# Kernel tuning notes

Measured on AMD Instinct MI355X. Metric: run time of the kernel, lower is better.

## Reference

```python
import jax, jax.numpy as jnp
import numpy as np

N = 100000   # num nodes
E = 500000   # num edges
F_IN = 128   # num_feats
H = 128      # dim_hidden
C = 40       # num_classes


def _glorot(key, fan_in, fan_out):
    lim = np.sqrt(6.0 / (fan_in + fan_out)).astype(np.float32)
    return jax.random.uniform(key, (fan_in, fan_out), jnp.float32, -lim, lim)


def setup_inputs() -> dict:
    key = jax.random.key(0)
    ks = jax.random.split(key, 8)
    x = jax.random.normal(ks[0], (N, F_IN), dtype=jnp.float32)
    edge_index = jax.random.randint(ks[1], (2, E), 0, N, dtype=jnp.int32)
    dims = [F_IN, H, H, H, C]  # num_layers = 4
    inp = {"x": x, "edge_index": edge_index}
    for i in range(4):
        inp[f"W{i}"] = _glorot(ks[2 + i], dims[i], dims[i + 1])
        inp[f"b{i}"] = jnp.zeros((dims[i + 1],), jnp.float32)
    return inp


def _gcn_norm(edge_index, num_nodes):
    # PyG gcn_norm: add self-loops (weight 1), symmetric D^-1/2 A D^-1/2
    loops = jnp.arange(num_nodes, dtype=edge_index.dtype)
    src = jnp.concatenate([edge_index[0], loops])
    dst = jnp.concatenate([edge_index[1], loops])
    deg = jax.ops.segment_sum(jnp.ones_like(src, jnp.float32), dst,
                              num_segments=num_nodes)
    dinv = jnp.where(deg > 0, jax.lax.rsqrt(deg), 0.0)
    norm = dinv[src] * dinv[dst]  # [E + N]
    return src, dst, norm


def _gcn_conv(h, W, b, src, dst, norm, num_nodes):
    h = h @ W                               # [N, out]
    msg = h[src] * norm[:, None]            # gather + scale, [E+N, out]
    agg = jax.ops.segment_sum(msg, dst, num_segments=num_nodes)
    return agg + b


def reference(x, edge_index, W0, b0, W1, b1, W2, b2, W3, b3):
    # eval mode: feature dropout and edge dropout (dropout_adj) are identity;
    # type_norm='None' -> no batchnorm.
    src, dst, norm = _gcn_norm(edge_index, N)
    Ws = [W0, W1, W2, W3]
    bs = [b0, b1, b2, b3]
    h = x
    for i in range(3):  # num_layers - 1 hidden layers with ReLU
        h = jax.nn.relu(_gcn_conv(h, Ws[i], bs[i], src, dst, norm, N))
    return _gcn_conv(h, Ws[3], bs[3], src, dst, norm, N)  # [N, C]
```

## Files before the change

kernel.cpp:

```cpp
#include <hip/hip_runtime.h>
#include <hip/hip_bf16.h>


#define F_DIM 128

#define SCAN_T 256
#define SCAN_I 8
#define SCAN_CHUNK (SCAN_T * SCAN_I)

typedef __attribute__((ext_vector_type(8))) short short8;
typedef __attribute__((ext_vector_type(4))) float f32x4;

__device__ __forceinline__ unsigned short f2bf_rne(float f) {
    unsigned int u = __float_as_uint(f);
    unsigned int r = (u + 0x7fffu + ((u >> 16) & 1u)) >> 16;
    return (unsigned short)r;
}

__global__ void count_dst_kernel(const int* __restrict__ dst, int* __restrict__ count, int E) {
    int e = blockIdx.x * blockDim.x + threadIdx.x;
    if (e < E) atomicAdd(&count[dst[e]], 1);
}

__global__ __launch_bounds__(SCAN_T) void scan_partial_kernel(const int* __restrict__ count,
                                                              int* __restrict__ blocksum, int n) {
    int b = blockIdx.x, t = threadIdx.x;
    int base = b * SCAN_CHUNK + t * SCAN_I;
    int s = 0;
#pragma unroll
    for (int j = 0; j < SCAN_I; ++j) {
        int i = base + j;
        if (i < n) s += count[i] + 1;
    }
    __shared__ int red[SCAN_T];
    red[t] = s;
    __syncthreads();
    for (int off = SCAN_T / 2; off > 0; off >>= 1) {
        if (t < off) red[t] += red[t + off];
        __syncthreads();
    }
    if (t == 0) blocksum[b] = red[0];
}

__global__ __launch_bounds__(1024) void scan_sums_kernel(const int* __restrict__ blocksum,
                                                         int* __restrict__ blockoff, int nb) {
    __shared__ int sums[1024];
    int t = threadIdx.x;
    sums[t] = (t < nb) ? blocksum[t] : 0;
    __syncthreads();
    for (int off = 1; off < 1024; off <<= 1) {
        int v = (t >= off) ? sums[t - off] : 0;
        __syncthreads();
        sums[t] += v;
        __syncthreads();
    }
    if (t < nb) blockoff[t] = (t == 0) ? 0 : sums[t - 1];
    if (t == 0) blockoff[nb] = sums[nb - 1];
}

__global__ __launch_bounds__(SCAN_T) void scan_write_fused_kernel(const int* __restrict__ count,
                                                                  const int* __restrict__ blockoff,
                                                                  int* __restrict__ rowptr,
                                                                  int* __restrict__ writepos,
                                                                  float* __restrict__ dinv,
                                                                  int* __restrict__ col,
                                                                  float* __restrict__ val,
                                                                  int n, int nb) {
    int b = blockIdx.x, t = threadIdx.x;
    int base = b * SCAN_CHUNK + t * SCAN_I;
    int c[SCAN_I];
    int s = 0;
#pragma unroll
    for (int j = 0; j < SCAN_I; ++j) {
        int i = base + j;
        c[j] = (i < n) ? count[i] + 1 : 0;
        s += c[j];
    }
    __shared__ int sums[SCAN_T];
    sums[t] = s;
    __syncthreads();
    for (int off = 1; off < SCAN_T; off <<= 1) {
        int v = (t >= off) ? sums[t - off] : 0;
        __syncthreads();
        sums[t] += v;
        __syncthreads();
    }
    int offset = blockoff[b] + ((t == 0) ? 0 : sums[t - 1]);
#pragma unroll
    for (int j = 0; j < SCAN_I; ++j) {
        int i = base + j;
        if (i < n) {
            rowptr[i] = offset;
            float d = rsqrtf((float)c[j]);
            dinv[i] = d;
            col[offset] = i;
            val[offset] = d * d;
            writepos[i] = offset + 1;
            offset += c[j];
        }
    }
    if (b == 0 && t == 0) rowptr[n] = blockoff[nb];
}

__global__ void fill_edges_kernel(const int* __restrict__ src, const int* __restrict__ dst,
                                  int* __restrict__ writepos, int* __restrict__ col,
                                  float* __restrict__ val, const float* __restrict__ dinv, int E) {
    int e = blockIdx.x * blockDim.x + threadIdx.x;
    if (e < E) {
        int s = src[e], d = dst[e];
        int p = atomicAdd(&writepos[d], 1);
        col[p] = s;
        val[p] = dinv[s] * dinv[d];
    }
}

__global__ __launch_bounds__(256) void cvt_bf16_kernel(const float* __restrict__ in,
                                                       unsigned short* __restrict__ out,
                                                       long nChunks) {
    long idx = (long)blockIdx.x * 256 + threadIdx.x;
    if (idx >= nChunks) return;
    const float4* in4 = (const float4*)in;
    float4 a = in4[idx * 2];
    float4 b = in4[idx * 2 + 1];
    uint4 o;
    o.x = (unsigned)f2bf_rne(a.x) | ((unsigned)f2bf_rne(a.y) << 16);
    o.y = (unsigned)f2bf_rne(a.z) | ((unsigned)f2bf_rne(a.w) << 16);
    o.z = (unsigned)f2bf_rne(b.x) | ((unsigned)f2bf_rne(b.y) << 16);
    o.w = (unsigned)f2bf_rne(b.z) | ((unsigned)f2bf_rne(b.w) << 16);
    ((uint4*)out)[idx] = o;
}

__global__ __launch_bounds__(256) void cvt_wt_kernel(const float* __restrict__ W,
                                                     unsigned short* __restrict__ WT) {
    int t = blockIdx.x * 256 + threadIdx.x;
    int k = t >> 7, c = t & 127;
    WT[(size_t)c * 128 + k] = f2bf_rne(W[(size_t)k * 128 + c]);
}

__global__ __launch_bounds__(256) void cvt_wt3_kernel(const float* __restrict__ W3,
                                                      unsigned short* __restrict__ WT3) {
    int t = blockIdx.x * 256 + threadIdx.x;
    if (t >= 48 * 128) return;
    int c = t >> 7, k = t & 127;
    WT3[(size_t)c * 128 + k] = (c < 40) ? f2bf_rne(W3[(size_t)k * 40 + c]) : (unsigned short)0;
}

__device__ __forceinline__ void acc8_bf16(float* acc, uint4 u, float v) {
    unsigned w[4] = {u.x, u.y, u.z, u.w};
#pragma unroll
    for (int i = 0; i < 4; ++i) {
        float lo = __uint_as_float(w[i] << 16);
        float hi = __uint_as_float(w[i] & 0xffff0000u);
        acc[2 * i] += v * lo;
        acc[2 * i + 1] += v * hi;
    }
}

__device__ __forceinline__ void gather_phase1(const int* __restrict__ rowptr,
                                              const int* __restrict__ col,
                                              const float* __restrict__ val,
                                              const uint4* __restrict__ H16,
                                              unsigned short (*aggb)[136], int n) {
    int m = threadIdx.x >> 3;
    int p = threadIdx.x & 7;
    int node = blockIdx.x * 32 + m;
    float acc[16];
#pragma unroll
    for (int q = 0; q < 16; ++q) acc[q] = 0.f;
    if (node < n) {
        int s = rowptr[node], e = rowptr[node + 1];
        int j = s;
        for (; j + 1 < e; j += 2) {
            int c0 = col[j], c1 = col[j + 1];
            float v0 = val[j], v1 = val[j + 1];
            const uint4* r0 = H16 + (size_t)c0 * 16 + p;
            const uint4* r1 = H16 + (size_t)c1 * 16 + p;
            uint4 a0 = r0[0], a1 = r0[8];
            uint4 b0 = r1[0], b1 = r1[8];
            acc8_bf16(acc + 0, a0, v0);
            acc8_bf16(acc + 8, a1, v0);
            acc8_bf16(acc + 0, b0, v1);
            acc8_bf16(acc + 8, b1, v1);
        }
        if (j < e) {
            int c0 = col[j];
            float v0 = val[j];
            const uint4* r0 = H16 + (size_t)c0 * 16 + p;
            uint4 a0 = r0[0], a1 = r0[8];
            acc8_bf16(acc + 0, a0, v0);
            acc8_bf16(acc + 8, a1, v0);
        }
    }
    short8 s0, s1;
#pragma unroll
    for (int q = 0; q < 8; ++q) s0[q] = (short)f2bf_rne(acc[q]);
#pragma unroll
    for (int q = 0; q < 8; ++q) s1[q] = (short)f2bf_rne(acc[8 + q]);
    *(short8*)&aggb[m][8 * p] = s0;
    *(short8*)&aggb[m][64 + 8 * p] = s1;
}

__global__ __launch_bounds__(256, 8) void fused_layer_mfma(const int* __restrict__ rowptr,
                                                           const int* __restrict__ col,
                                                           const float* __restrict__ val,
                                                           const unsigned short* __restrict__ Hin,
                                                           const unsigned short* __restrict__ WT,
                                                           const float* __restrict__ bias,
                                                           unsigned short* __restrict__ Hout,
                                                           int n) {
    __shared__ unsigned short aggb[32][136];
    gather_phase1(rowptr, col, val, (const uint4*)Hin, aggb, n);
    __syncthreads();

    int lane = threadIdx.x & 63;
    int wv = threadIdx.x >> 6;
    int l15 = lane & 15;
    int lg = lane >> 4;

    f32x4 a00 = {0.f, 0.f, 0.f, 0.f}, a01 = a00, a10 = a00, a11 = a00;

#pragma unroll
    for (int kc = 0; kc < 4; ++kc) {
        int ko = kc * 32 + lg * 8;
        short8 fa0 = *(const short8*)&aggb[l15][ko];
        short8 fa1 = *(const short8*)&aggb[l15 + 16][ko];
        short8 fb0 = *(const short8*)&WT[(size_t)(wv * 32 + l15) * 128 + ko];
        short8 fb1 = *(const short8*)&WT[(size_t)(wv * 32 + 16 + l15) * 128 + ko];
        a00 = __builtin_amdgcn_mfma_f32_16x16x32_bf16(fa0, fb0, a00, 0, 0, 0);
        a01 = __builtin_amdgcn_mfma_f32_16x16x32_bf16(fa0, fb1, a01, 0, 0, 0);
        a10 = __builtin_amdgcn_mfma_f32_16x16x32_bf16(fa1, fb0, a10, 0, 0, 0);
        a11 = __builtin_amdgcn_mfma_f32_16x16x32_bf16(fa1, fb1, a11, 0, 0, 0);
    }

    int base = blockIdx.x * 32;
#pragma unroll
    for (int nt = 0; nt < 2; ++nt) {
        int c = wv * 32 + nt * 16 + l15;
        float bv = bias[c];
#pragma unroll
        for (int mt = 0; mt < 2; ++mt) {
            f32x4 acc = (mt == 0) ? (nt == 0 ? a00 : a01) : (nt == 0 ? a10 : a11);
#pragma unroll
            for (int r = 0; r < 4; ++r) {
                int node = base + mt * 16 + lg * 4 + r;
                if (node < n) {
                    float o = fmaxf(acc[r] + bv, 0.f);
                    Hout[(size_t)node * 128 + c] = f2bf_rne(o);
                }
            }
        }
    }
}

__global__ __launch_bounds__(256, 8) void fused_layer_mfma_w3(const int* __restrict__ rowptr,
                                                              const int* __restrict__ col,
                                                              const float* __restrict__ val,
                                                              const unsigned short* __restrict__ Hin,
                                                              const unsigned short* __restrict__ WT,
                                                              const float* __restrict__ bias,
                                                              const unsigned short* __restrict__ WT3,
                                                              unsigned short* __restrict__ hw3,
                                                              int n) {
    __shared__ unsigned short aggb[32][136];
    gather_phase1(rowptr, col, val, (const uint4*)Hin, aggb, n);
    __syncthreads();

    int lane = threadIdx.x & 63;
    int wv = threadIdx.x >> 6;
    int l15 = lane & 15;
    int lg = lane >> 4;

    f32x4 a00 = {0.f, 0.f, 0.f, 0.f}, a01 = a00, a10 = a00, a11 = a00;

#pragma unroll
    for (int kc = 0; kc < 4; ++kc) {
        int ko = kc * 32 + lg * 8;
        short8 fa0 = *(const short8*)&aggb[l15][ko];
        short8 fa1 = *(const short8*)&aggb[l15 + 16][ko];
        short8 fb0 = *(const short8*)&WT[(size_t)(wv * 32 + l15) * 128 + ko];
        short8 fb1 = *(const short8*)&WT[(size_t)(wv * 32 + 16 + l15) * 128 + ko];
        a00 = __builtin_amdgcn_mfma_f32_16x16x32_bf16(fa0, fb0, a00, 0, 0, 0);
        a01 = __builtin_amdgcn_mfma_f32_16x16x32_bf16(fa0, fb1, a01, 0, 0, 0);
        a10 = __builtin_amdgcn_mfma_f32_16x16x32_bf16(fa1, fb0, a10, 0, 0, 0);
        a11 = __builtin_amdgcn_mfma_f32_16x16x32_bf16(fa1, fb1, a11, 0, 0, 0);
    }

    __syncthreads();
#pragma unroll
    for (int nt = 0; nt < 2; ++nt) {
        int c = wv * 32 + nt * 16 + l15;
        float bv = bias[c];
#pragma unroll
        for (int mt = 0; mt < 2; ++mt) {
            f32x4 acc = (mt == 0) ? (nt == 0 ? a00 : a01) : (nt == 0 ? a10 : a11);
#pragma unroll
            for (int r = 0; r < 4; ++r) {
                int row = mt * 16 + lg * 4 + r;
                aggb[row][c] = f2bf_rne(fmaxf(acc[r] + bv, 0.f));
            }
        }
    }
    __syncthreads();

    if (wv < 3) {
        f32x4 c0 = {0.f, 0.f, 0.f, 0.f}, c1 = c0;
#pragma unroll
        for (int kc = 0; kc < 4; ++kc) {
            int ko = kc * 32 + lg * 8;
            short8 fa0 = *(const short8*)&aggb[l15][ko];
            short8 fa1 = *(const short8*)&aggb[l15 + 16][ko];
            short8 fb = *(const short8*)&WT3[(size_t)(wv * 16 + l15) * 128 + ko];
            c0 = __builtin_amdgcn_mfma_f32_16x16x32_bf16(fa0, fb, c0, 0, 0, 0);
            c1 = __builtin_amdgcn_mfma_f32_16x16x32_bf16(fa1, fb, c1, 0, 0, 0);
        }
        int ccol = wv * 16 + l15;
        if (ccol < 40) {
            int base = blockIdx.x * 32;
#pragma unroll
            for (int mt = 0; mt < 2; ++mt) {
                f32x4 acc = (mt == 0) ? c0 : c1;
#pragma unroll
                for (int r = 0; r < 4; ++r) {
                    int node = base + mt * 16 + lg * 4 + r;
                    if (node < n) hw3[(size_t)node * 40 + ccol] = f2bf_rne(acc[r]);
                }
            }
        }
    }
}

__global__ __launch_bounds__(256, 8) void gather40_bf16_kernel(const int* __restrict__ rowptr,
                                                               const int* __restrict__ col,
                                                               const float* __restrict__ val,
                                                               const unsigned short* __restrict__ hw3,
                                                               const float* __restrict__ bias,
                                                               float* __restrict__ out, int n) {
    int m = threadIdx.x >> 3;
    int p = threadIdx.x & 7;
    int node = blockIdx.x * 32 + m;
    if (node >= n) return;

    float a0x = 0.f, a0y = 0.f, a0z = 0.f, a0w = 0.f;
    float a1x = 0.f, a1y = 0.f, a1z = 0.f, a1w = 0.f;

    int s = rowptr[node], e = rowptr[node + 1];
    for (int j = s; j < e; ++j) {
        int c0 = col[j];
        float v0 = val[j];
        const uint2* r0 = (const uint2*)(hw3 + (size_t)c0 * 40);
        uint2 u = r0[p];
        a0x += v0 * __uint_as_float(u.x << 16);
        a0y += v0 * __uint_as_float(u.x & 0xffff0000u);
        a0z += v0 * __uint_as_float(u.y << 16);
        a0w += v0 * __uint_as_float(u.y & 0xffff0000u);
        if (p < 2) {
            uint2 w = r0[8 + p];
            a1x += v0 * __uint_as_float(w.x << 16);
            a1y += v0 * __uint_as_float(w.x & 0xffff0000u);
            a1z += v0 * __uint_as_float(w.y << 16);
            a1w += v0 * __uint_as_float(w.y & 0xffff0000u);
        }
    }

    const float4* bi = (const float4*)bias;
    float4 bv = bi[p];
    float4 o0;
    o0.x = a0x + bv.x; o0.y = a0y + bv.y;
    o0.z = a0z + bv.z; o0.w = a0w + bv.w;
    ((float4*)(out + (size_t)node * 40))[p] = o0;
    if (p < 2) {
        float4 bw = bi[8 + p];
        float4 o1;
        o1.x = a1x + bw.x; o1.y = a1y + bw.y;
        o1.z = a1z + bw.z; o1.w = a1w + bw.w;
        ((float4*)(out + (size_t)node * 40))[8 + p] = o1;
    }
}

extern "C" void kernel_launch(void* const* d_in, const int* in_sizes, int n_in,
                              void* d_out, int out_size, void* d_ws, size_t ws_size,
                              hipStream_t stream) {
    const float* x = (const float*)d_in[0];
    const int* edge_index = (const int*)d_in[1];
    const float* W0 = (const float*)d_in[2];
    const float* b0 = (const float*)d_in[3];
    const float* W1 = (const float*)d_in[4];
    const float* b1 = (const float*)d_in[5];
    const float* W2 = (const float*)d_in[6];
    const float* b2 = (const float*)d_in[7];
    const float* W3 = (const float*)d_in[8];
    const float* b3 = (const float*)d_in[9];

    const int E = in_sizes[1] / 2;
    const int N = in_sizes[0] / F_DIM;
    const int NNZ = E + N;
    const int NB = (N + SCAN_CHUNK - 1) / SCAN_CHUNK;

    const int* src = edge_index;
    const int* dst = edge_index + E;

    char* ws = (char*)d_ws;
    size_t off = 0;
    auto carve = [&](size_t bytes) -> void* {
        void* p = ws + off;
        off = (off + bytes + 255) & ~(size_t)255;
        return p;
    };
    unsigned short* hbA = (unsigned short*)carve((size_t)N * F_DIM * sizeof(unsigned short));
    unsigned short* hbB = (unsigned short*)carve((size_t)N * F_DIM * sizeof(unsigned short));
    unsigned short* hw3 = (unsigned short*)carve((size_t)N * 40 * sizeof(unsigned short));
    unsigned short* WT0 = (unsigned short*)carve(128 * 128 * sizeof(unsigned short));
    unsigned short* WT1 = (unsigned short*)carve(128 * 128 * sizeof(unsigned short));
    unsigned short* WT2 = (unsigned short*)carve(128 * 128 * sizeof(unsigned short));
    unsigned short* WT3 = (unsigned short*)carve(48 * 128 * sizeof(unsigned short));
    int* count = (int*)carve((size_t)N * sizeof(int));
    float* dinv = (float*)carve((size_t)N * sizeof(float));
    int* rowptr = (int*)carve((size_t)(N + 1) * sizeof(int));
    int* writepos = (int*)carve((size_t)N * sizeof(int));
    int* colbuf = (int*)carve((size_t)NNZ * sizeof(int));
    float* valbuf = (float*)carve((size_t)NNZ * sizeof(float));
    int* blocksum = (int*)carve((size_t)NB * sizeof(int));
    int* blockoff = (int*)carve((size_t)(NB + 1) * sizeof(int));
    (void)ws_size;

    hipMemsetAsync(count, 0, (size_t)N * sizeof(int), stream);
    count_dst_kernel<<<(E + 255) / 256, 256, 0, stream>>>(dst, count, E);
    {
        long nChunks = (long)N * F_DIM / 8;
        cvt_bf16_kernel<<<(int)((nChunks + 255) / 256), 256, 0, stream>>>(x, hbA, nChunks);
    }
    cvt_wt_kernel<<<64, 256, 0, stream>>>(W0, WT0);
    cvt_wt_kernel<<<64, 256, 0, stream>>>(W1, WT1);
    cvt_wt_kernel<<<64, 256, 0, stream>>>(W2, WT2);
    cvt_wt3_kernel<<<24, 256, 0, stream>>>(W3, WT3);
    scan_partial_kernel<<<NB, SCAN_T, 0, stream>>>(count, blocksum, N);
    scan_sums_kernel<<<1, 1024, 0, stream>>>(blocksum, blockoff, NB);
    scan_write_fused_kernel<<<NB, SCAN_T, 0, stream>>>(count, blockoff, rowptr, writepos,
                                                       dinv, colbuf, valbuf, N, NB);
    fill_edges_kernel<<<(E + 255) / 256, 256, 0, stream>>>(src, dst, writepos, colbuf, valbuf, dinv, E);

    int nblk32 = (N + 31) / 32;
    fused_layer_mfma<<<nblk32, 256, 0, stream>>>(rowptr, colbuf, valbuf, hbA, WT0, b0, hbB, N);
    fused_layer_mfma<<<nblk32, 256, 0, stream>>>(rowptr, colbuf, valbuf, hbB, WT1, b1, hbA, N);
    fused_layer_mfma_w3<<<nblk32, 256, 0, stream>>>(rowptr, colbuf, valbuf, hbA, WT2, b2, WT3, hw3, N);

    gather40_bf16_kernel<<<nblk32, 256, 0, stream>>>(rowptr, colbuf, valbuf, hw3, b3, (float*)d_out, N);
}
```

Baseline: 242.8 us.

## Merge weight conversion launches, unroll gather loops deeper, relax launch bounds

Combines the four weight transpose/convert kernels into one launch to cut launch overhead. Unrolls the edge gather loop by four in the fused layer kernels and by two in the final 40-wide gather, so more independent row loads are in flight per thread. Lowers the min-blocks hint from 8 to 6 to give the compiler more registers for the wider unroll, at the cost of possibly lower occupancy.

```diff
diff --git a/kernel.cpp b/kernel.cpp
--- a/kernel.cpp
+++ b/kernel.cpp
@@ -130,19 +130,29 @@
     ((uint4*)out)[idx] = o;
 }
 
-__global__ __launch_bounds__(256) void cvt_wt_kernel(const float* __restrict__ W,
-                                                     unsigned short* __restrict__ WT) {
+__global__ __launch_bounds__(256) void cvt_weights_kernel(const float* __restrict__ W0,
+                                                          const float* __restrict__ W1,
+                                                          const float* __restrict__ W2,
+                                                          const float* __restrict__ W3,
+                                                          unsigned short* __restrict__ WT0,
+                                                          unsigned short* __restrict__ WT1,
+                                                          unsigned short* __restrict__ WT2,
+                                                          unsigned short* __restrict__ WT3) {
     int t = blockIdx.x * 256 + threadIdx.x;
-    int k = t >> 7, c = t & 127;
-    WT[(size_t)c * 128 + k] = f2bf_rne(W[(size_t)k * 128 + c]);
-}
-
-__global__ __launch_bounds__(256) void cvt_wt3_kernel(const float* __restrict__ W3,
-                                                      unsigned short* __restrict__ WT3) {
-    int t = blockIdx.x * 256 + threadIdx.x;
-    if (t >= 48 * 128) return;
-    int c = t >> 7, k = t & 127;
-    WT3[(size_t)c * 128 + k] = (c < 40) ? f2bf_rne(W3[(size_t)k * 40 + c]) : (unsigned short)0;
+    if (t < 3 * 16384) {
+        int w = t >> 14, i = t & 16383;
+        int k = i >> 7, c = i & 127;
+        const float* W = (w == 0) ? W0 : (w == 1) ? W1 : W2;
+        unsigned short* WT = (w == 0) ? WT0 : (w == 1) ? WT1 : WT2;
+        WT[(size_t)c * 128 + k] = f2bf_rne(W[(size_t)k * 128 + c]);
+    } else {
+        int i = t - 3 * 16384;
+        if (i < 48 * 128) {
+            int c = i >> 7, k = i & 127;
+            WT3[(size_t)c * 128 + k] = (c < 40) ? f2bf_rne(W3[(size_t)k * 40 + c])
+                                                : (unsigned short)0;
+        }
+    }
 }
 
 __device__ __forceinline__ void acc8_bf16(float* acc, uint4 u, float v) {
@@ -170,6 +180,26 @@
     if (node < n) {
         int s = rowptr[node], e = rowptr[node + 1];
         int j = s;
+        for (; j + 3 < e; j += 4) {
+            int c0 = col[j], c1 = col[j + 1], c2 = col[j + 2], c3 = col[j + 3];
+            float v0 = val[j], v1 = val[j + 1], v2 = val[j + 2], v3 = val[j + 3];
+            const uint4* r0 = H16 + (size_t)c0 * 16 + p;
+            const uint4* r1 = H16 + (size_t)c1 * 16 + p;
+            const uint4* r2 = H16 + (size_t)c2 * 16 + p;
+            const uint4* r3 = H16 + (size_t)c3 * 16 + p;
+            uint4 a0 = r0[0], a1 = r0[8];
+            uint4 b0 = r1[0], b1 = r1[8];
+            uint4 g0 = r2[0], g1 = r2[8];
+            uint4 d0 = r3[0], d1 = r3[8];
+            acc8_bf16(acc + 0, a0, v0);
+            acc8_bf16(acc + 8, a1, v0);
+            acc8_bf16(acc + 0, b0, v1);
+            acc8_bf16(acc + 8, b1, v1);
+            acc8_bf16(acc + 0, g0, v2);
+            acc8_bf16(acc + 8, g1, v2);
+            acc8_bf16(acc + 0, d0, v3);
+            acc8_bf16(acc + 8, d1, v3);
+        }
         for (; j + 1 < e; j += 2) {
             int c0 = col[j], c1 = col[j + 1];
             float v0 = val[j], v1 = val[j + 1];
@@ -200,7 +230,7 @@
     *(short8*)&aggb[m][64 + 8 * p] = s1;
 }
 
-__global__ __launch_bounds__(256, 8) void fused_layer_mfma(const int* __restrict__ rowptr,
+__global__ __launch_bounds__(256, 6) void fused_layer_mfma(const int* __restrict__ rowptr,
                                                            const int* __restrict__ col,
                                                            const float* __restrict__ val,
                                                            const unsigned short* __restrict__ Hin,
@@ -252,7 +282,7 @@
     }
 }
 
-__global__ __launch_bounds__(256, 8) void fused_layer_mfma_w3(const int* __restrict__ rowptr,
+__global__ __launch_bounds__(256, 6) void fused_layer_mfma_w3(const int* __restrict__ rowptr,
                                                               const int* __restrict__ col,
                                                               const float* __restrict__ val,
                                                               const unsigned short* __restrict__ Hin,
@@ -344,7 +374,26 @@
     float a1x = 0.f, a1y = 0.f, a1z = 0.f, a1w = 0.f;
 
     int s = rowptr[node], e = rowptr[node + 1];
-    for (int j = s; j < e; ++j) {
+    int j = s;
+    for (; j + 1 < e; j += 2) {
+        int c0 = col[j], c1 = col[j + 1];
+        float v0 = val[j], v1 = val[j + 1];
+        const uint2* r0 = (const uint2*)(hw3 + (size_t)c0 * 40);
+        const uint2* r1 = (const uint2*)(hw3 + (size_t)c1 * 40);
+        uint2 u0 = r0[p], u1 = r1[p];
+        a0x += v0 * __uint_as_float(u0.x << 16) + v1 * __uint_as_float(u1.x << 16);
+        a0y += v0 * __uint_as_float(u0.x & 0xffff0000u) + v1 * __uint_as_float(u1.x & 0xffff0000u);
+        a0z += v0 * __uint_as_float(u0.y << 16) + v1 * __uint_as_float(u1.y << 16);
+        a0w += v0 * __uint_as_float(u0.y & 0xffff0000u) + v1 * __uint_as_float(u1.y & 0xffff0000u);
+        if (p < 2) {
+            uint2 w0 = r0[8 + p], w1 = r1[8 + p];
+            a1x += v0 * __uint_as_float(w0.x << 16) + v1 * __uint_as_float(w1.x << 16);
+            a1y += v0 * __uint_as_float(w0.x & 0xffff0000u) + v1 * __uint_as_float(w1.x & 0xffff0000u);
+            a1z += v0 * __uint_as_float(w0.y << 16) + v1 * __uint_as_float(w1.y << 16);
+            a1w += v0 * __uint_as_float(w0.y & 0xffff0000u) + v1 * __uint_as_float(w1.y & 0xffff0000u);
+        }
+    }
+    if (j < e) {
         int c0 = col[j];
         float v0 = val[j];
         const uint2* r0 = (const uint2*)(hw3 + (size_t)c0 * 40);
@@ -429,10 +478,8 @@
         long nChunks = (long)N * F_DIM / 8;
         cvt_bf16_kernel<<<(int)((nChunks + 255) / 256), 256, 0, stream>>>(x, hbA, nChunks);
     }
-    cvt_wt_kernel<<<64, 256, 0, stream>>>(W0, WT0);
-    cvt_wt_kernel<<<64, 256, 0, stream>>>(W1, WT1);
-    cvt_wt_kernel<<<64, 256, 0, stream>>>(W2, WT2);
-    cvt_wt3_kernel<<<24, 256, 0, stream>>>(W3, WT3);
+    cvt_weights_kernel<<<(3 * 16384 + 48 * 128 + 255) / 256, 256, 0, stream>>>(
+        W0, W1, W2, W3, WT0, WT1, WT2, WT3);
     scan_partial_kernel<<<NB, SCAN_T, 0, stream>>>(count, blocksum, N);
     scan_sums_kernel<<<1, 1024, 0, stream>>>(blocksum, blockoff, NB);
     scan_write_fused_kernel<<<NB, SCAN_T, 0, stream>>>(count, blockoff, rowptr, writepos,
```

Result: slower. 257.5 us (+6.1%).
